# Performance work log

Measured on AMD Instinct MI355X. Metric: run time of the kernel, lower is better.

## Reference

```python
import jax, jax.numpy as jnp
import numpy as np

N_NODES = 50000
N_EDGES = 800000
BASIS = 64
HIDDEN_RO = 128
N_GRAPHS = 512
T = 3


def setup_inputs() -> dict:
    key = jax.random.key(0)
    ks = jax.random.split(key, 12)
    Z = jax.random.randint(ks[0], (N_NODES,), 0, 10)
    edge_index = jax.random.randint(ks[1], (2, N_EDGES), 0, N_NODES)
    edge_attr = jax.random.normal(ks[2], (N_EDGES, BASIS), dtype=jnp.float32)
    batch = jnp.sort(jax.random.randint(ks[3], (N_NODES,), 0, N_GRAPHS))
    s = 1.0 / np.sqrt(BASIS)
    embed = jax.random.normal(ks[4], (10, BASIS), dtype=jnp.float32)
    cfW = jax.random.uniform(ks[5], (BASIS, BASIS), jnp.float32, -s, s)
    cfb = jax.random.uniform(ks[6], (BASIS,), jnp.float32, -s, s)
    dfW = jax.random.uniform(ks[7], (BASIS, BASIS), jnp.float32, -s, s)
    dfb = jax.random.uniform(ks[8], (BASIS,), jnp.float32, -s, s)
    fcW = jax.random.uniform(ks[9], (BASIS, BASIS), jnp.float32, -s, s)  # no bias
    W1 = jax.random.uniform(ks[10], (BASIS, HIDDEN_RO), jnp.float32, -s, s)
    b1 = jnp.zeros((HIDDEN_RO,), jnp.float32)
    W2 = jax.random.uniform(ks[11], (HIDDEN_RO, 4), jnp.float32, -1.0 / np.sqrt(HIDDEN_RO), 1.0 / np.sqrt(HIDDEN_RO))
    b2 = jnp.zeros((4,), jnp.float32)
    return {"Z": Z, "edge_index": edge_index, "edge_attr": edge_attr, "batch": batch,
            "embed": embed, "cfW": cfW, "cfb": cfb, "dfW": dfW, "dfb": dfb, "fcW": fcW,
            "W1": W1, "b1": b1, "W2": W2, "b2": b2}


def reference(Z, edge_index, edge_attr, batch, embed, cfW, cfb, dfW, dfb, fcW, W1, b1, W2, b2):
    src, dst = edge_index[0], edge_index[1]  # x_j gathered from src, aggregated at dst
    C = embed[Z]  # [N, basis]
    # df(edge_attr) does not depend on C; compute once (same math, shared weights)
    d_feat = edge_attr @ dfW + dfb  # [E, basis]
    for _ in range(T):
        c_feat = C[src] @ cfW + cfb            # gather + linear  [E, basis]
        msg = jnp.tanh((c_feat * d_feat) @ fcW)  # [E, basis]
        agg = jax.ops.segment_sum(msg, dst, num_segments=N_NODES)
        C = C + agg
    h = jnp.tanh(C @ W1 + b1) @ W2 + b2        # readout MLP [N, 4]
    return jax.ops.segment_sum(h, batch, num_segments=N_GRAPHS)  # global_add_pool [G, 4]
```

## Files before the change

kernel.cpp:

```cpp
#include <hip/hip_runtime.h>
#include <math.h>

#define N_NODES   50000
#define N_EDGES   800000
#define BASIS     64
#define HIDDEN_RO 128
#define N_GRAPHS  512
#define T_ITERS   3
#define NB_SCAN   ((N_NODES + 255) / 256)

typedef short s8 __attribute__((ext_vector_type(8)));
typedef float f4 __attribute__((ext_vector_type(4)));

#define MFMA16(a, b, c) __builtin_amdgcn_mfma_f32_16x16x32_bf16(a, b, c, 0, 0, 0)

__device__ __forceinline__ float fast_tanh(float x) {
    float e = __expf(2.0f * x);
    return 1.0f - 2.0f / (e + 1.0f);
}

__device__ __forceinline__ f4 splat4(float x) { f4 v; v[0]=x; v[1]=x; v[2]=x; v[3]=x; return v; }

__device__ __forceinline__ void split8(const float* x, s8& hi, s8& lo) {
    union { unsigned a[4]; s8 v; } H, L;
    #pragma unroll
    for (int j = 0; j < 4; ++j) {
        float e0 = x[2*j], e1 = x[2*j+1];
        unsigned u0 = __float_as_uint(e0), u1 = __float_as_uint(e1);
        H.a[j] = (u0 >> 16) | (u1 & 0xFFFF0000u);
        float l0 = e0 - __uint_as_float(u0 & 0xFFFF0000u);
        float l1 = e1 - __uint_as_float(u1 & 0xFFFF0000u);
        L.a[j] = (__float_as_uint(l0) >> 16) | (__float_as_uint(l1) & 0xFFFF0000u);
    }
    hi = H.v; lo = L.v;
}

__device__ __forceinline__ void packW_dev(const float* __restrict__ W, s8* __restrict__ img, int t) {
    int lane = t & 63, q = lane >> 4, c = lane & 15;
    int f0 = (t >> 6) * 2;
    #pragma unroll
    for (int f = f0; f < f0 + 2; ++f) {
        int ks = f >> 2, g = f & 3;
        float tv[8];
        #pragma unroll
        for (int j = 0; j < 8; ++j)
            tv[j] = W[(ks*32 + q*8 + j) * 64 + g*16 + c];
        s8 hi, lo;
        split8(tv, hi, lo);
        img[f * 64 + lane]       = hi;
        img[(8 + f) * 64 + lane] = lo;
    }
}

__device__ __forceinline__ void packW1_dev(const float* __restrict__ W, s8* __restrict__ img, int t) {
    int lane = t & 63, q = lane >> 4, c = lane & 15;
    int f0 = (t >> 6) * 4;
    #pragma unroll
    for (int f = f0; f < f0 + 4; ++f) {
        int ks = f >> 3, g = f & 7;
        float tv[8];
        #pragma unroll
        for (int j = 0; j < 8; ++j)
            tv[j] = W[(ks*32 + q*8 + j) * HIDDEN_RO + g*16 + c];
        s8 hi, lo;
        split8(tv, hi, lo);
        img[f * 64 + lane]        = hi;
        img[(16 + f) * 64 + lane] = lo;
    }
}

__global__ void k_packW(const float* __restrict__ W0, const float* __restrict__ W1m,
                        const float* __restrict__ W2m, const float* __restrict__ W1ro,
                        s8* __restrict__ i0, s8* __restrict__ i1, s8* __restrict__ i2,
                        s8* __restrict__ i3) {
    int b = blockIdx.x, t = threadIdx.x;
    if (b == 0) packW_dev(W0, i0, t);
    else if (b == 1) packW_dev(W1m, i1, t);
    else if (b == 2) packW_dev(W2m, i2, t);
    else packW1_dev(W1ro, i3, t);
}

__global__ void k_init_hist(const int* __restrict__ Z, const float* __restrict__ embed,
                            float* __restrict__ C, const int* __restrict__ dst,
                            int* __restrict__ deg) {
    int i = blockIdx.x * blockDim.x + threadIdx.x;
    if (i < N_NODES * BASIS) { int n = i >> 6, c = i & 63; C[i] = embed[Z[n] * 64 + c]; }
    if (i < N_EDGES) atomicAdd(&deg[dst[i]], 1);
}

__global__ void k_scan1(const int* __restrict__ deg, int* __restrict__ off,
                        int* __restrict__ bsum) {
    __shared__ int ws[4];
    int b = blockIdx.x, t = threadIdx.x, lane = t & 63, w = t >> 6;
    int i = b * 256 + t;
    int v = (i < N_NODES) ? deg[i] : 0;
    int s = v;
    #pragma unroll
    for (int ofs = 1; ofs < 64; ofs <<= 1) {
        int tmp = __shfl_up(s, ofs, 64);
        if (lane >= ofs) s += tmp;
    }
    if (lane == 63) ws[w] = s;
    __syncthreads();
    if (t == 0) {
        int a = 0;
        #pragma unroll
        for (int k = 0; k < 4; ++k) { int x = ws[k]; ws[k] = a; a += x; }
        bsum[b] = a;
    }
    __syncthreads();
    int excl = ws[w] + s - v;
    if (i < N_NODES) off[i] = excl;
}

__global__ void k_scan2(int* __restrict__ bsum) {
    __shared__ int ws[4];
    int t = threadIdx.x, lane = t & 63, w = t >> 6;
    int v = (t < NB_SCAN) ? bsum[t] : 0;
    int s = v;
    #pragma unroll
    for (int ofs = 1; ofs < 64; ofs <<= 1) {
        int tmp = __shfl_up(s, ofs, 64);
        if (lane >= ofs) s += tmp;
    }
    if (lane == 63) ws[w] = s;
    __syncthreads();
    if (t == 0) {
        int a = 0;
        #pragma unroll
        for (int k = 0; k < 4; ++k) { int x = ws[k]; ws[k] = a; a += x; }
    }
    __syncthreads();
    int excl = ws[w] + s - v;
    if (t < NB_SCAN) bsum[t] = excl;
}

__global__ void k_scan3(const int* __restrict__ deg, int* __restrict__ off,
                        const int* __restrict__ bsum, int* __restrict__ cursor) {
    int b = blockIdx.x, i = b * 256 + threadIdx.x;
    if (i < N_NODES) {
        int val = off[i] + bsum[b];
        off[i] = val;
        cursor[i] = val;
        if (i == N_NODES - 1) off[N_NODES] = val + deg[i];
    }
}

__global__ void k_fill(const int* __restrict__ src, const int* __restrict__ dst,
                       int* __restrict__ cursor, int* __restrict__ slot_e,
                       int* __restrict__ slot_s) {
    int e = blockIdx.x * blockDim.x + threadIdx.x;
    if (e < N_EDGES) {
        int d = dst[e], s = src[e];
        int p = atomicAdd(&cursor[d], 1);
        slot_e[p] = e;
        slot_s[p] = s;
    }
}

template <int MODE>
__global__ __launch_bounds__(256, 4) void k_gemm64L(const float* __restrict__ in,
        const s8* __restrict__ wimg, const float* __restrict__ b,
        const int* __restrict__ slot_e, float* __restrict__ out, int rows) {
    __shared__ s8 LW[1024];
    int t = threadIdx.x;
    for (int i = t; i < 1024; i += 256) LW[i] = wimg[i];
    __syncthreads();
    int lane = t & 63, wv = t >> 6, q = lane >> 4, c = lane & 15;
    float bias[4];
    #pragma unroll
    for (int g = 0; g < 4; ++g) bias[g] = b[g*16 + c];
    int chunks = (rows + 15) >> 4;
    int wave = blockIdx.x * 4 + wv, nw = gridDim.x * 4;
    for (int ch = wave; ch < chunks; ch += nw) {
        int base = ch << 4;
        int row = base + c;
        bool valid = row < rows;
        int r = valid ? row : 0;
        if (MODE == 1) r = slot_e[valid ? row : base];
        const float4* ip = (const float4*)(in + (size_t)r * 64);
        s8 ahi[2], alo[2];
        #pragma unroll
        for (int ks = 0; ks < 2; ++ks) {
            float4 a0 = ip[ks*8 + q*2 + 0];
            float4 a1 = ip[ks*8 + q*2 + 1];
            float xs[8] = {a0.x,a0.y,a0.z,a0.w, a1.x,a1.y,a1.z,a1.w};
            if (!valid) {
                #pragma unroll
                for (int j = 0; j < 8; ++j) xs[j] = 0.0f;
            }
            split8(xs, ahi[ks], alo[ks]);
        }
        f4 acc[4];
        #pragma unroll
        for (int g = 0; g < 4; ++g) acc[g] = splat4(bias[g]);
        #pragma unroll
        for (int ks = 0; ks < 2; ++ks)
            #pragma unroll
            for (int g = 0; g < 4; ++g) {
                s8 wh = LW[(ks*4 + g) * 64 + lane];
                s8 wl = LW[(8 + ks*4 + g) * 64 + lane];
                acc[g] = MFMA16(ahi[ks], wh, acc[g]);
                acc[g] = MFMA16(ahi[ks], wl, acc[g]);
                acc[g] = MFMA16(alo[ks], wh, acc[g]);
            }
        #pragma unroll
        for (int g = 0; g < 4; ++g)
            #pragma unroll
            for (int r2 = 0; r2 < 4; ++r2) {
                int ro = base + q*4 + r2;
                if (ro < rows) out[(size_t)ro * 64 + g*16 + c] = acc[g][r2];
            }
    }
}

__global__ __launch_bounds__(256, 4) void k_mp5(const float* __restrict__ CF,
        const float* __restrict__ DF, const s8* __restrict__ wimg,
        const int* __restrict__ slot_s, const int* __restrict__ off,
        float* __restrict__ C) {
    __shared__ s8 LW[1024];
    int t = threadIdx.x;
    for (int i = t; i < 1024; i += 256) LW[i] = wimg[i];
    __syncthreads();
    int lane = t & 63, wv = t >> 6, q = lane >> 4, c = lane & 15;
    int wave = blockIdx.x * 4 + wv, nw = gridDim.x * 4;
    for (int n = wave; n < N_NODES; n += nw) {
        int beg = off[n], end = off[n + 1];
        if (beg >= end) continue;
        float acc0 = 0.f, acc1 = 0.f, acc2 = 0.f, acc3 = 0.f;
        int sl0 = beg + c; if (sl0 >= end) sl0 = end - 1;
        int srcn = slot_s[sl0];
        #pragma unroll 1
        for (int base = beg; base < end; base += 16) {
            int slot = base + c;
            bool valid = slot < end;
            if (!valid) slot = end - 1;
            int scur = srcn;
            if (base + 16 < end) {
                int s2 = base + 16 + c; if (s2 >= end) s2 = end - 1;
                srcn = slot_s[s2];
            }
            const float4* dp = (const float4*)(DF + (size_t)slot * 64);
            float4 d0 = dp[q*2],     d1 = dp[q*2 + 1];
            float4 d2 = dp[8 + q*2], d3 = dp[8 + q*2 + 1];
            const float4* cp = (const float4*)(CF + (size_t)scur * 64);
            float4 c0 = cp[q*2],     c1 = cp[q*2 + 1];
            float4 c2 = cp[8 + q*2], c3 = cp[8 + q*2 + 1];
            s8 ahi[2], alo[2];
            {
                float xs[8] = {c0.x*d0.x, c0.y*d0.y, c0.z*d0.z, c0.w*d0.w,
                               c1.x*d1.x, c1.y*d1.y, c1.z*d1.z, c1.w*d1.w};
                if (!valid) {
                    #pragma unroll
                    for (int j = 0; j < 8; ++j) xs[j] = 0.0f;
                }
                split8(xs, ahi[0], alo[0]);
                float ys[8] = {c2.x*d2.x, c2.y*d2.y, c2.z*d2.z, c2.w*d2.w,
                               c3.x*d3.x, c3.y*d3.y, c3.z*d3.z, c3.w*d3.w};
                if (!valid) {
                    #pragma unroll
                    for (int j = 0; j < 8; ++j) ys[j] = 0.0f;
                }
                split8(ys, ahi[1], alo[1]);
            }
            f4 d[4];
            #pragma unroll
            for (int g = 0; g < 4; ++g) d[g] = splat4(0.0f);
            #pragma unroll
            for (int ks = 0; ks < 2; ++ks)
                #pragma unroll
                for (int g = 0; g < 4; ++g) {
                    s8 wh = LW[(ks*4 + g) * 64 + lane];
                    s8 wl = LW[(8 + ks*4 + g) * 64 + lane];
                    d[g] = MFMA16(ahi[ks], wh, d[g]);
                    d[g] = MFMA16(ahi[ks], wl, d[g]);
                    d[g] = MFMA16(alo[ks], wh, d[g]);
                }
            acc0 += fast_tanh(d[0][0]) + fast_tanh(d[0][1]) + fast_tanh(d[0][2]) + fast_tanh(d[0][3]);
            acc1 += fast_tanh(d[1][0]) + fast_tanh(d[1][1]) + fast_tanh(d[1][2]) + fast_tanh(d[1][3]);
            acc2 += fast_tanh(d[2][0]) + fast_tanh(d[2][1]) + fast_tanh(d[2][2]) + fast_tanh(d[2][3]);
            acc3 += fast_tanh(d[3][0]) + fast_tanh(d[3][1]) + fast_tanh(d[3][2]) + fast_tanh(d[3][3]);
        }
        acc0 += __shfl_xor(acc0, 16, 64); acc0 += __shfl_xor(acc0, 32, 64);
        acc1 += __shfl_xor(acc1, 16, 64); acc1 += __shfl_xor(acc1, 32, 64);
        acc2 += __shfl_xor(acc2, 16, 64); acc2 += __shfl_xor(acc2, 32, 64);
        acc3 += __shfl_xor(acc3, 16, 64); acc3 += __shfl_xor(acc3, 32, 64);
        float v = (q == 0) ? acc0 : (q == 1) ? acc1 : (q == 2) ? acc2 : acc3;
        C[(size_t)n * 64 + lane] += v;
    }
}

__global__ __launch_bounds__(256) void k_gemm64_fb(const float* __restrict__ in,
        const float* __restrict__ W, const float* __restrict__ b,
        float* __restrict__ out, int rows) {
    int r = blockIdx.x * blockDim.x + threadIdx.x;
    if (r >= rows) return;
    float acc[BASIS];
    #pragma unroll
    for (int c = 0; c < BASIS; ++c) acc[c] = b[c];
    const float4* in4 = (const float4*)(in + (size_t)r * BASIS);
    #pragma unroll 1
    for (int k0 = 0; k0 < 16; ++k0) {
        float4 xv = in4[k0];
        #pragma unroll
        for (int c = 0; c < BASIS; ++c)
            acc[c] += xv.x * W[(4*k0+0)*64+c] + xv.y * W[(4*k0+1)*64+c]
                    + xv.z * W[(4*k0+2)*64+c] + xv.w * W[(4*k0+3)*64+c];
    }
    #pragma unroll
    for (int c = 0; c < BASIS; ++c) out[(size_t)r * BASIS + c] = acc[c];
}
__global__ __launch_bounds__(256) void k_edge_fb(const float* __restrict__ CF,
        const float* __restrict__ ea, const float* __restrict__ dfW,
        const float* __restrict__ dfb, const float* __restrict__ fcW,
        const int* __restrict__ src, const int* __restrict__ dst,
        float* __restrict__ C) {
    int e = blockIdx.x * blockDim.x + threadIdx.x;
    if (e >= N_EDGES) return;
    int s = src[e], d = dst[e];
    float dfeat[BASIS];
    #pragma unroll
    for (int c = 0; c < BASIS; ++c) dfeat[c] = dfb[c];
    const float4* ea4 = (const float4*)(ea + (size_t)e * BASIS);
    #pragma unroll
    for (int k0 = 0; k0 < 16; ++k0) {
        float4 xv = ea4[k0];
        #pragma unroll
        for (int c = 0; c < BASIS; ++c)
            dfeat[c] += xv.x * dfW[(4*k0+0)*64+c] + xv.y * dfW[(4*k0+1)*64+c]
                      + xv.z * dfW[(4*k0+2)*64+c] + xv.w * dfW[(4*k0+3)*64+c];
    }
    const float4* cf4 = (const float4*)(CF + (size_t)s * BASIS);
    float acc[BASIS];
    #pragma unroll
    for (int c = 0; c < BASIS; ++c) acc[c] = 0.0f;
    #pragma unroll
    for (int k0 = 0; k0 < 16; ++k0) {
        float4 a = cf4[k0];
        float x0 = a.x * dfeat[4*k0+0], x1 = a.y * dfeat[4*k0+1];
        float x2 = a.z * dfeat[4*k0+2], x3 = a.w * dfeat[4*k0+3];
        #pragma unroll
        for (int c = 0; c < BASIS; ++c)
            acc[c] += x0 * fcW[(4*k0+0)*64+c] + x1 * fcW[(4*k0+1)*64+c]
                    + x2 * fcW[(4*k0+2)*64+c] + x3 * fcW[(4*k0+3)*64+c];
    }
    float* crow = C + (size_t)d * BASIS;
    #pragma unroll
    for (int c = 0; c < BASIS; ++c) atomicAdd(&crow[c], fast_tanh(acc[c]));
}

__global__ __launch_bounds__(256) void k_readout2(const float* __restrict__ C,
        const float* __restrict__ W1, const float* __restrict__ b1,
        const float* __restrict__ W2, const float* __restrict__ b2,
        const int* __restrict__ batch, float* __restrict__ out) {
    __shared__ float w1[BASIS * HIDDEN_RO];
    __shared__ float xbuf[4][64];
    int t = threadIdx.x;
    for (int i = t; i < BASIS * HIDDEN_RO; i += 256) w1[i] = W1[i];
    __syncthreads();
    int lane = t & 63, wv = t >> 6;
    float b1a = b1[lane], b1b = b1[64 + lane];
    float4 w2a = ((const float4*)W2)[lane];
    float4 w2b = ((const float4*)W2)[64 + lane];
    int wave = blockIdx.x * 4 + wv;
    int nw   = gridDim.x * 4;
    for (int n = wave; n < N_NODES; n += nw) {
        float x = C[(size_t)n * 64 + lane];
        xbuf[wv][lane] = x;
        __builtin_amdgcn_wave_barrier();
        const float4* xb = (const float4*)xbuf[wv];
        float sa = b1a, sb = b1b;
        #pragma unroll
        for (int k4 = 0; k4 < 16; ++k4) {
            float4 xv = xb[k4];
            const float* r0 = &w1[(4*k4 + 0) * HIDDEN_RO];
            const float* r1 = &w1[(4*k4 + 1) * HIDDEN_RO];
            const float* r2 = &w1[(4*k4 + 2) * HIDDEN_RO];
            const float* r3 = &w1[(4*k4 + 3) * HIDDEN_RO];
            sa += xv.x * r0[lane]      + xv.y * r1[lane]
                + xv.z * r2[lane]      + xv.w * r3[lane];
            sb += xv.x * r0[64 + lane] + xv.y * r1[64 + lane]
                + xv.z * r2[64 + lane] + xv.w * r3[64 + lane];
        }
        float ha = fast_tanh(sa), hb = fast_tanh(sb);
        float v0 = ha * w2a.x + hb * w2b.x;
        float v1 = ha * w2a.y + hb * w2b.y;
        float v2 = ha * w2a.z + hb * w2b.z;
        float v3 = ha * w2a.w + hb * w2b.w;
        #pragma unroll
        for (int ofs = 32; ofs >= 1; ofs >>= 1) {
            v0 += __shfl_down(v0, ofs, 64);
            v1 += __shfl_down(v1, ofs, 64);
            v2 += __shfl_down(v2, ofs, 64);
            v3 += __shfl_down(v3, ofs, 64);
        }
        if (lane == 0) {
            int g = batch[n];
            atomicAdd(&out[(size_t)g * 4 + 0], v0);
            atomicAdd(&out[(size_t)g * 4 + 1], v1);
            atomicAdd(&out[(size_t)g * 4 + 2], v2);
            atomicAdd(&out[(size_t)g * 4 + 3], v3);
        }
        __builtin_amdgcn_wave_barrier();
    }
}

__global__ __launch_bounds__(256, 2) void k_readout3(const float* __restrict__ C,
        const s8* __restrict__ wimg, const float* __restrict__ b1,
        const float* __restrict__ W2, const float* __restrict__ b2,
        const int* __restrict__ batch, float* __restrict__ out) {
    __shared__ s8 LW[2048];
    int t = threadIdx.x;
    for (int i = t; i < 2048; i += 256) LW[i] = wimg[i];
    __syncthreads();
    int lane = t & 63, wv = t >> 6, q = lane >> 4, c = lane & 15;
    float bias[8];
    #pragma unroll
    for (int g = 0; g < 8; ++g) bias[g] = b1[g*16 + c];
    f4 w2r[8];
    #pragma unroll
    for (int g = 0; g < 8; ++g) {
        float4 w4 = ((const float4*)W2)[g*16 + c];
        w2r[g][0] = w4.x; w2r[g][1] = w4.y; w2r[g][2] = w4.z; w2r[g][3] = w4.w;
    }
    float4 b2v = *(const float4*)b2;
    int chunks = (N_NODES + 15) >> 4;
    int wave = blockIdx.x * 4 + wv, nw = gridDim.x * 4;
    for (int ch = wave; ch < chunks; ch += nw) {
        int base = ch << 4;
        int row = base + c;
        bool valid = row < N_NODES;
        int r = valid ? row : 0;
        const float4* ip = (const float4*)(C + (size_t)r * 64);
        s8 ahi[2], alo[2];
        #pragma unroll
        for (int ks = 0; ks < 2; ++ks) {
            float4 a0 = ip[ks*8 + q*2 + 0];
            float4 a1 = ip[ks*8 + q*2 + 1];
            float xs[8] = {a0.x,a0.y,a0.z,a0.w, a1.x,a1.y,a1.z,a1.w};
            if (!valid) {
                #pragma unroll
                for (int j = 0; j < 8; ++j) xs[j] = 0.0f;
            }
            split8(xs, ahi[ks], alo[ks]);
        }
        f4 acc[8];
        #pragma unroll
        for (int g = 0; g < 8; ++g) acc[g] = splat4(bias[g]);
        #pragma unroll
        for (int ks = 0; ks < 2; ++ks)
            #pragma unroll
            for (int g = 0; g < 8; ++g) {
                s8 wh = LW[(ks*8 + g) * 64 + lane];
                s8 wl = LW[(16 + ks*8 + g) * 64 + lane];
                acc[g] = MFMA16(ahi[ks], wh, acc[g]);
                acc[g] = MFMA16(ahi[ks], wl, acc[g]);
                acc[g] = MFMA16(alo[ks], wh, acc[g]);
            }
        f4 v4[4];
        #pragma unroll
        for (int r2 = 0; r2 < 4; ++r2) v4[r2] = splat4(0.0f);
        #pragma unroll
        for (int g = 0; g < 8; ++g)
            #pragma unroll
            for (int r2 = 0; r2 < 4; ++r2) {
                float h = fast_tanh(acc[g][r2]);
                #pragma unroll
                for (int j = 0; j < 4; ++j) v4[r2][j] += h * w2r[g][j];
            }
        #pragma unroll
        for (int r2 = 0; r2 < 4; ++r2)
            #pragma unroll
            for (int j = 0; j < 4; ++j) {
                float x = v4[r2][j];
                x += __shfl_xor(x, 1, 64);
                x += __shfl_xor(x, 2, 64);
                x += __shfl_xor(x, 4, 64);
                x += __shfl_xor(x, 8, 64);
                v4[r2][j] = x;
            }
        if (c == 0) {
            #pragma unroll
            for (int r2 = 0; r2 < 4; ++r2) {
                int ro = base + q*4 + r2;
                if (ro < N_NODES) {
                    int g_id = batch[ro];
                    atomicAdd(&out[(size_t)g_id * 4 + 0], v4[r2][0] + b2v.x);
                    atomicAdd(&out[(size_t)g_id * 4 + 1], v4[r2][1] + b2v.y);
                    atomicAdd(&out[(size_t)g_id * 4 + 2], v4[r2][2] + b2v.z);
                    atomicAdd(&out[(size_t)g_id * 4 + 3], v4[r2][3] + b2v.w);
                }
            }
        }
    }
}

extern "C" void kernel_launch(void* const* d_in, const int* in_sizes, int n_in,
                              void* d_out, int out_size, void* d_ws, size_t ws_size,
                              hipStream_t stream) {
    const int*   Z     = (const int*)d_in[0];
    const int*   ei    = (const int*)d_in[1];
    const float* ea    = (const float*)d_in[2];
    const int*   batch = (const int*)d_in[3];
    const float* embed = (const float*)d_in[4];
    const float* cfW   = (const float*)d_in[5];
    const float* cfb   = (const float*)d_in[6];
    const float* dfW   = (const float*)d_in[7];
    const float* dfb   = (const float*)d_in[8];
    const float* fcW   = (const float*)d_in[9];
    const float* W1    = (const float*)d_in[10];
    const float* b1    = (const float*)d_in[11];
    const float* W2    = (const float*)d_in[12];
    const float* b2    = (const float*)d_in[13];
    const int* src = ei;
    const int* dst = ei + N_EDGES;
    float* out = (float*)d_out;

    const size_t bC = (size_t)N_NODES * BASIS * sizeof(float);
    const size_t bE = (size_t)N_EDGES * sizeof(int);
    const size_t bO = (size_t)(N_NODES + 1) * sizeof(int);
    const size_t bI = 1024 * sizeof(s8);
    char* p = (char*)d_ws;
    float* C      = (float*)p;  p += bC;
    float* CF     = (float*)p;  p += bC;
    int*   slotE  = (int*)p;    p += bE;
    int*   slotS  = (int*)p;    p += bE;
    int*   deg    = (int*)p;    p += bO;
    int*   off    = (int*)p;    p += bO;
    int*   cursor = (int*)p;    p += bO;
    p = (char*)(((uintptr_t)p + 255) & ~(uintptr_t)255);
    s8* imgDF = (s8*)p;  p += bI;
    s8* imgCF = (s8*)p;  p += bI;
    s8* imgFC = (s8*)p;  p += bI;
    s8* imgW1 = (s8*)p;  p += 2048 * sizeof(s8);
    int* bsum = (int*)p; p += 256 * sizeof(int);
    float* DF = (float*)p;
    const size_t need = (size_t)(p - (char*)d_ws) + (size_t)N_EDGES * BASIS * sizeof(float);
    const bool full = ws_size >= need;

    hipMemsetAsync(d_out, 0, (size_t)out_size * sizeof(float), stream);

    if (full) {
        hipMemsetAsync(deg, 0, bO, stream);
        k_init_hist<<<(N_NODES * BASIS + 255) / 256, 256, 0, stream>>>(Z, embed, C, dst, deg);
        k_packW<<<4, 256, 0, stream>>>(dfW, cfW, fcW, W1, imgDF, imgCF, imgFC, imgW1);
        k_scan1<<<NB_SCAN, 256, 0, stream>>>(deg, off, bsum);
        k_scan2<<<1, 256, 0, stream>>>(bsum);
        k_scan3<<<NB_SCAN, 256, 0, stream>>>(deg, off, bsum, cursor);
        k_fill<<<(N_EDGES + 255) / 256, 256, 0, stream>>>(src, dst, cursor, slotE, slotS);
        k_gemm64L<1><<<4096, 256, 0, stream>>>(ea, imgDF, dfb, slotE, DF, N_EDGES);
        for (int t = 0; t < T_ITERS; ++t) {
            k_gemm64L<0><<<800, 256, 0, stream>>>(C, imgCF, cfb, nullptr, CF, N_NODES);
            k_mp5<<<2048, 256, 0, stream>>>(CF, DF, imgFC, slotS, off, C);
        }
        k_readout3<<<1024, 256, 0, stream>>>(C, imgW1, b1, W2, b2, batch, out);
    } else {
        k_init_hist<<<(N_NODES * BASIS + 255) / 256, 256, 0, stream>>>(Z, embed, C, dst, (int*)CF);
        for (int t = 0; t < T_ITERS; ++t) {
            k_gemm64_fb<<<(N_NODES + 255) / 256, 256, 0, stream>>>(C, cfW, cfb, CF, N_NODES);
            k_edge_fb<<<(N_EDGES + 255) / 256, 256, 0, stream>>>(CF, ea, dfW, dfb, fcW, src, dst, C);
        }
        k_readout2<<<512, 256, 0, stream>>>(C, W1, b1, W2, b2, batch, out);
    }
}
```

Baseline: 866.0 us.

## Prefetch next chunk in GEMM and message-passing loops; scatter DF writes instead of gathering

The edge-feature GEMM now reads edge_attr rows in order and scatters its output rows to CSR slot positions. Before, it gathered input rows through slot_e. k_fill now records each edge's slot instead of each slot's edge. Both the GEMM and the message-passing kernel software-pipeline their loads, fetching the next chunk's rows (and the next node's offsets) while computing the current one, which hides global-memory latency. The cost is higher register pressure, which could reduce occupancy under launch_bounds(256,4).

```diff
diff --git a/kernel.cpp b/kernel.cpp
--- a/kernel.cpp
+++ b/kernel.cpp
@@ -147,21 +147,21 @@
 }
 
 __global__ void k_fill(const int* __restrict__ src, const int* __restrict__ dst,
-                       int* __restrict__ cursor, int* __restrict__ slot_e,
-                       int* __restrict__ slot_s) {
+                       int* __restrict__ cursor, int* __restrict__ slot_s,
+                       int* __restrict__ slot_p) {
     int e = blockIdx.x * blockDim.x + threadIdx.x;
     if (e < N_EDGES) {
         int d = dst[e], s = src[e];
         int p = atomicAdd(&cursor[d], 1);
-        slot_e[p] = e;
         slot_s[p] = s;
+        slot_p[e] = p;
     }
 }
 
 template <int MODE>
 __global__ __launch_bounds__(256, 4) void k_gemm64L(const float* __restrict__ in,
         const s8* __restrict__ wimg, const float* __restrict__ b,
-        const int* __restrict__ slot_e, float* __restrict__ out, int rows) {
+        const int* __restrict__ map, float* __restrict__ out, int rows) {
     __shared__ s8 LW[1024];
     int t = threadIdx.x;
     for (int i = t; i < 1024; i += 256) LW[i] = wimg[i];
@@ -172,24 +172,49 @@
     for (int g = 0; g < 4; ++g) bias[g] = b[g*16 + c];
     int chunks = (rows + 15) >> 4;
     int wave = blockIdx.x * 4 + wv, nw = gridDim.x * 4;
-    for (int ch = wave; ch < chunks; ch += nw) {
+    int ch = wave;
+    if (ch >= chunks) return;
+    float4 a0, a1, a2, a3; bool valA;
+    {
+        int base = ch << 4, row = base + c;
+        valA = row < rows;
+        int r = valA ? row : 0;
+        const float4* ip = (const float4*)(in + (size_t)r * 64);
+        a0 = ip[q*2]; a1 = ip[q*2+1]; a2 = ip[8+q*2]; a3 = ip[8+q*2+1];
+    }
+    #pragma unroll 1
+    while (ch < chunks) {
+        int chn = ch + nw;
+        float4 b0, b1, b2, b3; bool valB = false;
+        if (chn < chunks) {
+            int base = chn << 4, row = base + c;
+            valB = row < rows;
+            int r = valB ? row : 0;
+            const float4* ip = (const float4*)(in + (size_t)r * 64);
+            b0 = ip[q*2]; b1 = ip[q*2+1]; b2 = ip[8+q*2]; b3 = ip[8+q*2+1];
+        }
         int base = ch << 4;
-        int row = base + c;
-        bool valid = row < rows;
-        int r = valid ? row : 0;
-        if (MODE == 1) r = slot_e[valid ? row : base];
-        const float4* ip = (const float4*)(in + (size_t)r * 64);
+        int orow[4];
+        #pragma unroll
+        for (int r2 = 0; r2 < 4; ++r2) {
+            int ro = base + q*4 + r2;
+            if (ro >= rows) ro = rows - 1;
+            orow[r2] = (MODE == 2) ? map[ro] : ro;
+        }
         s8 ahi[2], alo[2];
-        #pragma unroll
-        for (int ks = 0; ks < 2; ++ks) {
-            float4 a0 = ip[ks*8 + q*2 + 0];
-            float4 a1 = ip[ks*8 + q*2 + 1];
+        {
             float xs[8] = {a0.x,a0.y,a0.z,a0.w, a1.x,a1.y,a1.z,a1.w};
-            if (!valid) {
+            if (!valA) {
                 #pragma unroll
                 for (int j = 0; j < 8; ++j) xs[j] = 0.0f;
             }
-            split8(xs, ahi[ks], alo[ks]);
+            split8(xs, ahi[0], alo[0]);
+            float ys[8] = {a2.x,a2.y,a2.z,a2.w, a3.x,a3.y,a3.z,a3.w};
+            if (!valA) {
+                #pragma unroll
+                for (int j = 0; j < 8; ++j) ys[j] = 0.0f;
+            }
+            split8(ys, ahi[1], alo[1]);
         }
         f4 acc[4];
         #pragma unroll
@@ -208,13 +233,55 @@
         for (int g = 0; g < 4; ++g)
             #pragma unroll
             for (int r2 = 0; r2 < 4; ++r2) {
-                int ro = base + q*4 + r2;
-                if (ro < rows) out[(size_t)ro * 64 + g*16 + c] = acc[g][r2];
-            }
-    }
-}
-
-__global__ __launch_bounds__(256, 4) void k_mp5(const float* __restrict__ CF,
+                if (base + q*4 + r2 < rows)
+                    out[(size_t)orow[r2] * 64 + g*16 + c] = acc[g][r2];
+            }
+        a0 = b0; a1 = b1; a2 = b2; a3 = b3; valA = valB;
+        ch = chn;
+    }
+}
+
+struct Ch { float4 d0, d1, d2, d3, c0, c1, c2, c3; int valid; };
+
+__device__ __forceinline__ void mp_compute(const Ch& ch, const s8* __restrict__ LW, int lane,
+        float& acc0, float& acc1, float& acc2, float& acc3) {
+    s8 ahi[2], alo[2];
+    {
+        float xs[8] = {ch.c0.x*ch.d0.x, ch.c0.y*ch.d0.y, ch.c0.z*ch.d0.z, ch.c0.w*ch.d0.w,
+                       ch.c1.x*ch.d1.x, ch.c1.y*ch.d1.y, ch.c1.z*ch.d1.z, ch.c1.w*ch.d1.w};
+        if (!ch.valid) {
+            #pragma unroll
+            for (int j = 0; j < 8; ++j) xs[j] = 0.0f;
+        }
+        split8(xs, ahi[0], alo[0]);
+        float ys[8] = {ch.c2.x*ch.d2.x, ch.c2.y*ch.d2.y, ch.c2.z*ch.d2.z, ch.c2.w*ch.d2.w,
+                       ch.c3.x*ch.d3.x, ch.c3.y*ch.d3.y, ch.c3.z*ch.d3.z, ch.c3.w*ch.d3.w};
+        if (!ch.valid) {
+            #pragma unroll
+            for (int j = 0; j < 8; ++j) ys[j] = 0.0f;
+        }
+        split8(ys, ahi[1], alo[1]);
+    }
+    f4 d[4];
+    #pragma unroll
+    for (int g = 0; g < 4; ++g) d[g] = splat4(0.0f);
+    #pragma unroll
+    for (int ks = 0; ks < 2; ++ks)
+        #pragma unroll
+        for (int g = 0; g < 4; ++g) {
+            s8 wh = LW[(ks*4 + g) * 64 + lane];
+            s8 wl = LW[(8 + ks*4 + g) * 64 + lane];
+            d[g] = MFMA16(ahi[ks], wh, d[g]);
+            d[g] = MFMA16(ahi[ks], wl, d[g]);
+            d[g] = MFMA16(alo[ks], wh, d[g]);
+        }
+    acc0 += fast_tanh(d[0][0]) + fast_tanh(d[0][1]) + fast_tanh(d[0][2]) + fast_tanh(d[0][3]);
+    acc1 += fast_tanh(d[1][0]) + fast_tanh(d[1][1]) + fast_tanh(d[1][2]) + fast_tanh(d[1][3]);
+    acc2 += fast_tanh(d[2][0]) + fast_tanh(d[2][1]) + fast_tanh(d[2][2]) + fast_tanh(d[2][3]);
+    acc3 += fast_tanh(d[3][0]) + fast_tanh(d[3][1]) + fast_tanh(d[3][2]) + fast_tanh(d[3][3]);
+}
+
+__global__ __launch_bounds__(256, 4) void k_mp6(const float* __restrict__ CF,
         const float* __restrict__ DF, const s8* __restrict__ wimg,
         const int* __restrict__ slot_s, const int* __restrict__ off,
         float* __restrict__ C) {
@@ -224,69 +291,65 @@
     __syncthreads();
     int lane = t & 63, wv = t >> 6, q = lane >> 4, c = lane & 15;
     int wave = blockIdx.x * 4 + wv, nw = gridDim.x * 4;
-    for (int n = wave; n < N_NODES; n += nw) {
-        int beg = off[n], end = off[n + 1];
-        if (beg >= end) continue;
-        float acc0 = 0.f, acc1 = 0.f, acc2 = 0.f, acc3 = 0.f;
-        int sl0 = beg + c; if (sl0 >= end) sl0 = end - 1;
-        int srcn = slot_s[sl0];
-        #pragma unroll 1
-        for (int base = beg; base < end; base += 16) {
-            int slot = base + c;
-            bool valid = slot < end;
-            if (!valid) slot = end - 1;
-            int scur = srcn;
-            if (base + 16 < end) {
-                int s2 = base + 16 + c; if (s2 >= end) s2 = end - 1;
-                srcn = slot_s[s2];
-            }
-            const float4* dp = (const float4*)(DF + (size_t)slot * 64);
-            float4 d0 = dp[q*2],     d1 = dp[q*2 + 1];
-            float4 d2 = dp[8 + q*2], d3 = dp[8 + q*2 + 1];
-            const float4* cp = (const float4*)(CF + (size_t)scur * 64);
-            float4 c0 = cp[q*2],     c1 = cp[q*2 + 1];
-            float4 c2 = cp[8 + q*2], c3 = cp[8 + q*2 + 1];
-            s8 ahi[2], alo[2];
+
+    int n = wave;
+    int beg = 0, end = 0;
+    if (n < N_NODES) { beg = off[n]; end = off[n + 1]; }
+    #pragma unroll 1
+    while (n < N_NODES) {
+        int n2 = n + nw;
+        int beg2 = 0, end2 = 0;
+        if (n2 < N_NODES) { beg2 = off[n2]; end2 = off[n2 + 1]; }
+        if (beg < end) {
+            float cprev = C[(size_t)n * 64 + lane];
+            float acc0 = 0.f, acc1 = 0.f, acc2 = 0.f, acc3 = 0.f;
+            int slA = beg + c;
+            int vA = slA < end;
+            if (!vA) slA = end - 1;
+            int sA = slot_s[slA];
+            Ch A;
             {
-                float xs[8] = {c0.x*d0.x, c0.y*d0.y, c0.z*d0.z, c0.w*d0.w,
-                               c1.x*d1.x, c1.y*d1.y, c1.z*d1.z, c1.w*d1.w};
-                if (!valid) {
-                    #pragma unroll
-                    for (int j = 0; j < 8; ++j) xs[j] = 0.0f;
+                const float4* dp = (const float4*)(DF + (size_t)slA * 64);
+                A.d0 = dp[q*2]; A.d1 = dp[q*2+1]; A.d2 = dp[8+q*2]; A.d3 = dp[8+q*2+1];
+                const float4* cp = (const float4*)(CF + (size_t)sA * 64);
+                A.c0 = cp[q*2]; A.c1 = cp[q*2+1]; A.c2 = cp[8+q*2]; A.c3 = cp[8+q*2+1];
+                A.valid = vA;
+            }
+            int snext = 0;
+            if (beg + 16 < end) {
+                int sl = beg + 16 + c; if (sl >= end) sl = end - 1;
+                snext = slot_s[sl];
+            }
+            int base = beg;
+            #pragma unroll 1
+            for (; base + 16 < end; base += 16) {
+                int slB = base + 16 + c;
+                int vB = slB < end;
+                if (!vB) slB = end - 1;
+                Ch B;
+                {
+                    const float4* dp = (const float4*)(DF + (size_t)slB * 64);
+                    B.d0 = dp[q*2]; B.d1 = dp[q*2+1]; B.d2 = dp[8+q*2]; B.d3 = dp[8+q*2+1];
+                    const float4* cp = (const float4*)(CF + (size_t)snext * 64);
+                    B.c0 = cp[q*2]; B.c1 = cp[q*2+1]; B.c2 = cp[8+q*2]; B.c3 = cp[8+q*2+1];
+                    B.valid = vB;
                 }
-                split8(xs, ahi[0], alo[0]);
-                float ys[8] = {c2.x*d2.x, c2.y*d2.y, c2.z*d2.z, c2.w*d2.w,
-                               c3.x*d3.x, c3.y*d3.y, c3.z*d3.z, c3.w*d3.w};
-                if (!valid) {
-                    #pragma unroll
-                    for (int j = 0; j < 8; ++j) ys[j] = 0.0f;
+                if (base + 32 < end) {
+                    int sl = base + 32 + c; if (sl >= end) sl = end - 1;
+                    snext = slot_s[sl];
                 }
-                split8(ys, ahi[1], alo[1]);
-            }
-            f4 d[4];
-            #pragma unroll
-            for (int g = 0; g < 4; ++g) d[g] = splat4(0.0f);
-            #pragma unroll
-            for (int ks = 0; ks < 2; ++ks)
-                #pragma unroll
-                for (int g = 0; g < 4; ++g) {
-                    s8 wh = LW[(ks*4 + g) * 64 + lane];
-                    s8 wl = LW[(8 + ks*4 + g) * 64 + lane];
-                    d[g] = MFMA16(ahi[ks], wh, d[g]);
-                    d[g] = MFMA16(ahi[ks], wl, d[g]);
-                    d[g] = MFMA16(alo[ks], wh, d[g]);
-                }
-            acc0 += fast_tanh(d[0][0]) + fast_tanh(d[0][1]) + fast_tanh(d[0][2]) + fast_tanh(d[0][3]);
-            acc1 += fast_tanh(d[1][0]) + fast_tanh(d[1][1]) + fast_tanh(d[1][2]) + fast_tanh(d[1][3]);
-            acc2 += fast_tanh(d[2][0]) + fast_tanh(d[2][1]) + fast_tanh(d[2][2]) + fast_tanh(d[2][3]);
-            acc3 += fast_tanh(d[3][0]) + fast_tanh(d[3][1]) + fast_tanh(d[3][2]) + fast_tanh(d[3][3]);
-        }
-        acc0 += __shfl_xor(acc0, 16, 64); acc0 += __shfl_xor(acc0, 32, 64);
-        acc1 += __shfl_xor(acc1, 16, 64); acc1 += __shfl_xor(acc1, 32, 64);
-        acc2 += __shfl_xor(acc2, 16, 64); acc2 += __shfl_xor(acc2, 32, 64);
-        acc3 += __shfl_xor(acc3, 16, 64); acc3 += __shfl_xor(acc3, 32, 64);
-        float v = (q == 0) ? acc0 : (q == 1) ? acc1 : (q == 2) ? acc2 : acc3;
-        C[(size_t)n * 64 + lane] += v;
+                mp_compute(A, LW, lane, acc0, acc1, acc2, acc3);
+                A = B;
+            }
+            mp_compute(A, LW, lane, acc0, acc1, acc2, acc3);
+            acc0 += __shfl_xor(acc0, 16, 64); acc0 += __shfl_xor(acc0, 32, 64);
+            acc1 += __shfl_xor(acc1, 16, 64); acc1 += __shfl_xor(acc1, 32, 64);
+            acc2 += __shfl_xor(acc2, 16, 64); acc2 += __shfl_xor(acc2, 32, 64);
+            acc3 += __shfl_xor(acc3, 16, 64); acc3 += __shfl_xor(acc3, 32, 64);
+            float v = (q == 0) ? acc0 : (q == 1) ? acc1 : (q == 2) ? acc2 : acc3;
+            C[(size_t)n * 64 + lane] = cprev + v;
+        }
+        n = n2; beg = beg2; end = end2;
     }
 }
 
@@ -523,7 +586,7 @@
     char* p = (char*)d_ws;
     float* C      = (float*)p;  p += bC;
     float* CF     = (float*)p;  p += bC;
-    int*   slotE  = (int*)p;    p += bE;
+    int*   slotP  = (int*)p;    p += bE;
     int*   slotS  = (int*)p;    p += bE;
     int*   deg    = (int*)p;    p += bO;
     int*   off    = (int*)p;    p += bO;
@@ -547,11 +610,11 @@
         k_scan1<<<NB_SCAN, 256, 0, stream>>>(deg, off, bsum);
         k_scan2<<<1, 256, 0, stream>>>(bsum);
         k_scan3<<<NB_SCAN, 256, 0, stream>>>(deg, off, bsum, cursor);
-        k_fill<<<(N_EDGES + 255) / 256, 256, 0, stream>>>(src, dst, cursor, slotE, slotS);
-        k_gemm64L<1><<<4096, 256, 0, stream>>>(ea, imgDF, dfb, slotE, DF, N_EDGES);
+        k_fill<<<(N_EDGES + 255) / 256, 256, 0, stream>>>(src, dst, cursor, slotS, slotP);
+        k_gemm64L<2><<<4096, 256, 0, stream>>>(ea, imgDF, dfb, slotP, DF, N_EDGES);
         for (int t = 0; t < T_ITERS; ++t) {
             k_gemm64L<0><<<800, 256, 0, stream>>>(C, imgCF, cfb, nullptr, CF, N_NODES);
-            k_mp5<<<2048, 256, 0, stream>>>(CF, DF, imgFC, slotS, off, C);
+            k_mp6<<<2048, 256, 0, stream>>>(CF, DF, imgFC, slotS, off, C);
         }
         k_readout3<<<1024, 256, 0, stream>>>(C, imgW1, b1, W2, b2, batch, out);
     } else {
```

New measurement: 1.014 ms. 1.17x slower.
